# Kernel tuning notes

Hardware: AMD Instinct MI355X
Metric: run time of the kernel (lower is better)

The kernel has to match this reference:

```python
import jax, jax.numpy as jnp
import numpy as np

TOPK = 2
SCALE = 32.0 / 16.0  # alpha / rank
EPS = 1e-20


def setup_inputs() -> dict:
    key = jax.random.key(0)
    ks = jax.random.split(key, 6)
    B, S, D = 4, 4096, 2048
    E, R, QO, VO = 8, 16, 2048, 2048
    return {
        "hidden_states": jax.random.normal(ks[0], (B, S, D), dtype=jnp.float32),
        "router_weight": jax.random.normal(ks[1], (E, D), dtype=jnp.float32) * 0.02,
        "q_lora_a": jax.random.normal(ks[2], (E, D, R), dtype=jnp.float32) * 0.02,
        "q_lora_b": jax.random.normal(ks[3], (E, R, QO), dtype=jnp.float32) * 0.02,
        "v_lora_a": jax.random.normal(ks[4], (E, D, R), dtype=jnp.float32) * 0.02,
        "v_lora_b": jax.random.normal(ks[5], (E, R, VO), dtype=jnp.float32) * 0.02,
    }


def reference(hidden_states, router_weight, q_lora_a, q_lora_b, v_lora_a, v_lora_b):
    orig_shape = hidden_states.shape[:-1]
    D = hidden_states.shape[-1]
    E = router_weight.shape[0]
    h = hidden_states.reshape(-1, D)                       # [T, D]

    # --- routing ---
    logits = h @ router_weight.T                           # [T, E]
    probs = jax.nn.softmax(logits, axis=-1)
    scores, idx = jax.lax.top_k(probs, TOPK)               # [T, K]
    scores = scores / (jnp.sum(scores, axis=-1, keepdims=True) + EPS)
    # dense per-expert combine weight (0 for unselected experts), incl. LoRA scale
    w = jnp.sum(jax.nn.one_hot(idx, E, dtype=h.dtype) * scores[..., None], axis=1) * SCALE  # [T, E]

    # --- grouped LoRA (dense over experts; E and rank are small) ---
    q_low = jnp.einsum('td,edr->ter', h, q_lora_a) * w[:, :, None]  # [T, E, R]
    v_low = jnp.einsum('td,edr->ter', h, v_lora_a) * w[:, :, None]
    q_delta = jnp.einsum('ter,erq->tq', q_low, q_lora_b)            # [T, QO]
    v_delta = jnp.einsum('ter,erv->tv', v_low, v_lora_b)            # [T, VO]

    return (q_delta.reshape(*orig_shape, q_delta.shape[-1]),
            v_delta.reshape(*orig_shape, v_delta.shape[-1]))
```

## Files before the change

kernel.cpp:

```cpp
#include <hip/hip_runtime.h>

#define T_TOKENS 16384
#define DIM 2048
#define NE 8
#define QOUT 2048
#define LSCALE 2.0f

typedef __attribute__((ext_vector_type(4))) float f32x4;
typedef __attribute__((ext_vector_type(8))) short s16x8;
typedef __attribute__((ext_vector_type(4))) short s16x4;

__device__ __forceinline__ short f2bf(float f) {
  unsigned u = __builtin_bit_cast(unsigned, f);
  u += 0x7fffu + ((u >> 16) & 1u);
  return (short)(u >> 16);
}

__device__ __forceinline__ void barrier_lds() {
  asm volatile("s_waitcnt lgkmcnt(0)" ::: "memory");
  __builtin_amdgcn_s_barrier();
}

__global__ __launch_bounds__(256) void k_pack(
    const float* __restrict__ qa, const float* __restrict__ qb,
    const float* __restrict__ va, const float* __restrict__ vb,
    short* __restrict__ Bq1, short* __restrict__ Bv1,
    short* __restrict__ Bq2, short* __restrict__ Bv2) {
  int tid = blockIdx.x * 256 + threadIdx.x;
  if (tid < 65536) {
    int mat = tid >> 15;
    int idx = tid & 32767;
    int d8 = idx >> 7, c = idx & 127;
    int e = c >> 4, r = c & 15;
    const float* src = mat ? va : qa;
    short* dst = mat ? Bv1 : Bq1;
    s16x8 v;
#pragma unroll
    for (int j = 0; j < 8; ++j)
      v[j] = f2bf(src[((size_t)e * DIM + d8 * 8 + j) * 16 + r]);
    *(s16x8*)(dst + (size_t)idx * 8) = v;
  } else {
    int t2 = tid - 65536;
    int mat = t2 >> 15;
    int idx = t2 & 32767;
    int k8 = idx >> 11, c = idx & 2047;
    const float* src = mat ? vb : qb;
    short* dst = mat ? Bv2 : Bq2;
    s16x8 v;
#pragma unroll
    for (int j = 0; j < 8; ++j)
      v[j] = f2bf(src[(size_t)(k8 * 8 + j) * QOUT + c]);
    *(s16x8*)(dst + (size_t)idx * 8) = v;
  }
}

__global__ __launch_bounds__(512) void k_fused(
    const float* __restrict__ h, const float* __restrict__ rw,
    const short* __restrict__ Bq1, const short* __restrict__ Bv1,
    const short* __restrict__ Bq2, const short* __restrict__ Bv2,
    float* __restrict__ out) {
  __shared__ short At[2][32][72];
  __shared__ short low[32][264];
  __shared__ float wl[32][NE];

  const int tid = threadIdx.x;
  const int lane = tid & 63, wv = tid >> 6;
  const int lrow = lane & 15, lk = lane >> 4;
  const int row0 = blockIdx.x * 32;
  const int r  = tid >> 4;
  const int kq = (tid & 15) * 4;

  const float* hrow = h + (size_t)(row0 + r) * DIM + kq;
  const short* B1 = (wv >= 4) ? Bv1 : Bq1;
  int cc2[2];
#pragma unroll
  for (int ct = 0; ct < 2; ++ct) cc2[ct] = (wv & 3) * 32 + ct * 16 + lrow;

  float4 hv0 = *(const float4*)(hrow);
  float4 hv1 = *(const float4*)(hrow + 64);

  float lg[NE] = {0.f, 0.f, 0.f, 0.f, 0.f, 0.f, 0.f, 0.f};
  f32x4 acc1[2][2] = {};

#pragma unroll 2
  for (int kb = 0; kb < DIM; kb += 64) {
    const int cur = (kb >> 6) & 1;
    float4 hv2 = *(const float4*)(hrow + ((kb + 128) & (DIM - 1)));
    s16x8 bA[2], bB[2];
#pragma unroll
    for (int ct = 0; ct < 2; ++ct) {
      int d8 = (kb >> 3) + lk;
      bA[ct] = *(const s16x8*)(B1 + ((size_t)d8 * 128 + cc2[ct]) * 8);
      bB[ct] = *(const s16x8*)(B1 + ((size_t)(d8 + 4) * 128 + cc2[ct]) * 8);
    }
    s16x4 hb4;
    hb4[0] = f2bf(hv0.x); hb4[1] = f2bf(hv0.y);
    hb4[2] = f2bf(hv0.z); hb4[3] = f2bf(hv0.w);
    *(s16x4*)&At[cur][r][kq] = hb4;
#pragma unroll
    for (int e = 0; e < NE; ++e) {
      float4 rv = *(const float4*)(rw + e * DIM + kb + kq);
      lg[e] += hv0.x * rv.x + hv0.y * rv.y + hv0.z * rv.z + hv0.w * rv.w;
    }
    barrier_lds();
    s16x8 a0[2], a1[2];
#pragma unroll
    for (int rt = 0; rt < 2; ++rt) {
      a0[rt] = *(const s16x8*)&At[cur][rt * 16 + lrow][lk * 8];
      a1[rt] = *(const s16x8*)&At[cur][rt * 16 + lrow][32 + lk * 8];
    }
#pragma unroll
    for (int rt = 0; rt < 2; ++rt)
#pragma unroll
      for (int ct = 0; ct < 2; ++ct) {
        acc1[rt][ct] = __builtin_amdgcn_mfma_f32_16x16x32_bf16(bA[ct], a0[rt], acc1[rt][ct], 0, 0, 0);
        acc1[rt][ct] = __builtin_amdgcn_mfma_f32_16x16x32_bf16(bB[ct], a1[rt], acc1[rt][ct], 0, 0, 0);
      }
    hv0 = hv1; hv1 = hv2;
  }

#pragma unroll
  for (int e = 0; e < NE; ++e) {
    lg[e] += __shfl_xor(lg[e], 1, 64);
    lg[e] += __shfl_xor(lg[e], 2, 64);
    lg[e] += __shfl_xor(lg[e], 4, 64);
    lg[e] += __shfl_xor(lg[e], 8, 64);
  }
  float mx = lg[0];
#pragma unroll
  for (int e = 1; e < NE; ++e) mx = fmaxf(mx, lg[e]);
  float p[NE], sum = 0.f;
#pragma unroll
  for (int e = 0; e < NE; ++e) { p[e] = expf(lg[e] - mx); sum += p[e]; }
  int i1 = 0; float v1 = p[0];
#pragma unroll
  for (int e = 1; e < NE; ++e) if (p[e] > v1) { v1 = p[e]; i1 = e; }
  float v2 = -1.f; int i2 = 0;
#pragma unroll
  for (int e = 0; e < NE; ++e) if (e != i1 && p[e] > v2) { v2 = p[e]; i2 = e; }
  float s1 = v1 / sum, s2 = v2 / sum;
  float dn = s1 + s2 + 1e-20f;
  float w1 = s1 / dn * LSCALE, w2 = s2 / dn * LSCALE;
  if ((tid & 15) < 8) {
    int el = tid & 7;
    wl[r][el] = (el == i1) ? w1 : ((el == i2) ? w2 : 0.f);
  }

  const int m = wv >> 2;
  const int cwave = (wv & 3) * 512;
  const short* B2 = m ? Bv2 : Bq2;
  s16x8 bc[4];
#pragma unroll
  for (int ct = 0; ct < 4; ++ct) {
    int c = cwave + ct * 16 + lrow;
    bc[ct] = *(const s16x8*)(B2 + ((size_t)lk * QOUT + c) * 8);
  }

  __syncthreads();
#pragma unroll
  for (int rt = 0; rt < 2; ++rt)
#pragma unroll
    for (int ct = 0; ct < 2; ++ct) {
      int tok = rt * 16 + lrow;
      float wgt = wl[tok][(wv & 3) * 2 + ct];
      s16x4 v;
#pragma unroll
      for (int j = 0; j < 4; ++j) v[j] = f2bf(acc1[rt][ct][j] * wgt);
      *(s16x4*)&low[tok][wv * 32 + ct * 16 + lk * 4] = v;
    }
  barrier_lds();

  float* op = out + (size_t)m * T_TOKENS * QOUT;
  s16x8 a2[2][4];
#pragma unroll
  for (int rt = 0; rt < 2; ++rt)
#pragma unroll
    for (int kk = 0; kk < 4; ++kk)
      a2[rt][kk] = *(const s16x8*)&low[rt * 16 + lrow][m * 128 + kk * 32 + lk * 8];

  f32x4 acc[2][4] = {};
#pragma unroll 4
  for (int it = 0; it < 32; ++it) {
    const int sub = it >> 2, kk = it & 3;
    const int itn = (it + 1) & 31;
    const int subn = itn >> 2, kkn = itn & 3;
    s16x8 bn[4];
#pragma unroll
    for (int ct = 0; ct < 4; ++ct) {
      int c = cwave + subn * 64 + ct * 16 + lrow;
      bn[ct] = *(const s16x8*)(B2 + ((size_t)(kkn * 4 + lk) * QOUT + c) * 8);
    }
#pragma unroll
    for (int rt = 0; rt < 2; ++rt)
#pragma unroll
      for (int ct = 0; ct < 4; ++ct)
        acc[rt][ct] = __builtin_amdgcn_mfma_f32_16x16x32_bf16(bc[ct], a2[rt][kk], acc[rt][ct], 0, 0, 0);
    if (kk == 3) {
      int cb = cwave + sub * 64;
#pragma unroll
      for (int rt = 0; rt < 2; ++rt)
#pragma unroll
        for (int ct = 0; ct < 4; ++ct) {
          int t = row0 + rt * 16 + lrow;
          int col = cb + ct * 16 + lk * 4;
          __builtin_nontemporal_store(acc[rt][ct], (f32x4*)(op + (size_t)t * QOUT + col));
          acc[rt][ct] = (f32x4){0.f, 0.f, 0.f, 0.f};
        }
    }
#pragma unroll
    for (int ct = 0; ct < 4; ++ct) bc[ct] = bn[ct];
  }
}

extern "C" void kernel_launch(void* const* d_in, const int* in_sizes, int n_in,
                              void* d_out, int out_size, void* d_ws, size_t ws_size,
                              hipStream_t stream) {
  const float* h  = (const float*)d_in[0];
  const float* rw = (const float*)d_in[1];
  const float* qa = (const float*)d_in[2];
  const float* qb = (const float*)d_in[3];
  const float* va = (const float*)d_in[4];
  const float* vb = (const float*)d_in[5];
  float* out = (float*)d_out;
  char* ws = (char*)d_ws;

  short* Bq1 = (short*)(ws);
  short* Bv1 = (short*)(ws + (512 << 10));
  short* Bq2 = (short*)(ws + (1024 << 10));
  short* Bv2 = (short*)(ws + (1536 << 10));

  k_pack<<<512, 256, 0, stream>>>(qa, qb, va, vb, Bq1, Bv1, Bq2, Bv2);
  k_fused<<<T_TOKENS / 32, 512, 0, stream>>>(h, rw, Bq1, Bv1, Bq2, Bv2, out);
}
```

Measured before the change: 140.9 us.

## Stage hidden states into LDS via async global_load_lds with triple buffering

Replaces the register-prefetched float4 loads of hidden states with direct global-to-LDS async loads into a three-deep, XOR-swizzled fp32 LDS buffer. The bf16 conversion now happens after reading from LDS, and a vmcnt(1) barrier keeps one load in flight. The aim is to free registers and overlap the h stream with the MFMA work. The B2 preload also moves after the low-rank write, and the loop is no longer unrolled, which may cost some instruction overlap.

```diff
diff --git a/kernel.cpp b/kernel.cpp
--- a/kernel.cpp
+++ b/kernel.cpp
@@ -16,8 +16,26 @@
   return (short)(u >> 16);
 }
 
+__device__ __forceinline__ s16x8 pack8(float4 a, float4 b) {
+  s16x8 r;
+  r[0] = f2bf(a.x); r[1] = f2bf(a.y); r[2] = f2bf(a.z); r[3] = f2bf(a.w);
+  r[4] = f2bf(b.x); r[5] = f2bf(b.y); r[6] = f2bf(b.z); r[7] = f2bf(b.w);
+  return r;
+}
+
+__device__ __forceinline__ void gload16(const void* g, void* l) {
+  __builtin_amdgcn_global_load_lds(
+      (const __attribute__((address_space(1))) void*)g,
+      (__attribute__((address_space(3))) void*)l, 16, 0, 0);
+}
+
 __device__ __forceinline__ void barrier_lds() {
   asm volatile("s_waitcnt lgkmcnt(0)" ::: "memory");
+  __builtin_amdgcn_s_barrier();
+}
+
+__device__ __forceinline__ void barrier_vm1() {
+  asm volatile("s_waitcnt vmcnt(1) lgkmcnt(0)" ::: "memory");
   __builtin_amdgcn_s_barrier();
 }
 
@@ -59,7 +77,7 @@
     const short* __restrict__ Bq1, const short* __restrict__ Bv1,
     const short* __restrict__ Bq2, const short* __restrict__ Bv2,
     float* __restrict__ out) {
-  __shared__ short At[2][32][72];
+  __shared__ float Ah[3][32][64];
   __shared__ short low[32][264];
   __shared__ float wl[32][NE];
 
@@ -67,56 +85,61 @@
   const int lane = tid & 63, wv = tid >> 6;
   const int lrow = lane & 15, lk = lane >> 4;
   const int row0 = blockIdx.x * 32;
-  const int r  = tid >> 4;
-  const int kq = (tid & 15) * 4;
-
-  const float* hrow = h + (size_t)(row0 + r) * DIM + kq;
+  const int g_r = tid >> 4;
+  const int g_s = tid & 15;
+  const int psw = (g_s ^ (g_r & 15));
+
   const short* B1 = (wv >= 4) ? Bv1 : Bq1;
   int cc2[2];
 #pragma unroll
   for (int ct = 0; ct < 2; ++ct) cc2[ct] = (wv & 3) * 32 + ct * 16 + lrow;
 
-  float4 hv0 = *(const float4*)(hrow);
-  float4 hv1 = *(const float4*)(hrow + 64);
+  const float* hsrc = h + (size_t)(row0 + g_r) * DIM + psw * 4;
+
+  gload16(hsrc, (char*)&Ah[0][0][0] + wv * 1024);
+  gload16(hsrc + 64, (char*)&Ah[1][0][0] + wv * 1024);
+  barrier_vm1();
 
   float lg[NE] = {0.f, 0.f, 0.f, 0.f, 0.f, 0.f, 0.f, 0.f};
   f32x4 acc1[2][2] = {};
-
-#pragma unroll 2
+  int cur = 0, nxt = 1, nx2 = 2;
+
+#pragma unroll 1
   for (int kb = 0; kb < DIM; kb += 64) {
-    const int cur = (kb >> 6) & 1;
-    float4 hv2 = *(const float4*)(hrow + ((kb + 128) & (DIM - 1)));
-    s16x8 bA[2], bB[2];
-#pragma unroll
-    for (int ct = 0; ct < 2; ++ct) {
-      int d8 = (kb >> 3) + lk;
-      bA[ct] = *(const s16x8*)(B1 + ((size_t)d8 * 128 + cc2[ct]) * 8);
-      bB[ct] = *(const s16x8*)(B1 + ((size_t)(d8 + 4) * 128 + cc2[ct]) * 8);
-    }
-    s16x4 hb4;
-    hb4[0] = f2bf(hv0.x); hb4[1] = f2bf(hv0.y);
-    hb4[2] = f2bf(hv0.z); hb4[3] = f2bf(hv0.w);
-    *(s16x4*)&At[cur][r][kq] = hb4;
-#pragma unroll
-    for (int e = 0; e < NE; ++e) {
-      float4 rv = *(const float4*)(rw + e * DIM + kb + kq);
-      lg[e] += hv0.x * rv.x + hv0.y * rv.y + hv0.z * rv.z + hv0.w * rv.w;
-    }
-    barrier_lds();
-    s16x8 a0[2], a1[2];
+    float4 hv = *(const float4*)&Ah[cur][g_r][psw * 4];
+#pragma unroll 1
+    for (int g = 0; g < 2; ++g) {
+#pragma unroll
+      for (int e = 0; e < 4; ++e) {
+        float4 rv = *(const float4*)(rw + (g * 4 + e) * DIM + kb + g_s * 4);
+        lg[g * 4 + e] += hv.x * rv.x + hv.y * rv.y + hv.z * rv.z + hv.w * rv.w;
+      }
+    }
+    s16x8 b[2][2];
+#pragma unroll
+    for (int hf = 0; hf < 2; ++hf)
+#pragma unroll
+      for (int ct = 0; ct < 2; ++ct) {
+        int d8 = (kb >> 3) + hf * 4 + lk;
+        b[hf][ct] = *(const s16x8*)(B1 + ((size_t)d8 * 128 + cc2[ct]) * 8);
+      }
 #pragma unroll
     for (int rt = 0; rt < 2; ++rt) {
-      a0[rt] = *(const s16x8*)&At[cur][rt * 16 + lrow][lk * 8];
-      a1[rt] = *(const s16x8*)&At[cur][rt * 16 + lrow][32 + lk * 8];
-    }
-#pragma unroll
-    for (int rt = 0; rt < 2; ++rt)
-#pragma unroll
-      for (int ct = 0; ct < 2; ++ct) {
-        acc1[rt][ct] = __builtin_amdgcn_mfma_f32_16x16x32_bf16(bA[ct], a0[rt], acc1[rt][ct], 0, 0, 0);
-        acc1[rt][ct] = __builtin_amdgcn_mfma_f32_16x16x32_bf16(bB[ct], a1[rt], acc1[rt][ct], 0, 0, 0);
+      const float* base = &Ah[cur][rt * 16 + lrow][0];
+#pragma unroll
+      for (int hf = 0; hf < 2; ++hf) {
+        int s0 = hf * 8 + lk * 2;
+        float4 f0 = *(const float4*)(base + ((s0 ^ lrow) * 4));
+        float4 f1 = *(const float4*)(base + (((s0 + 1) ^ lrow) * 4));
+        s16x8 a = pack8(f0, f1);
+#pragma unroll
+        for (int ct = 0; ct < 2; ++ct)
+          acc1[rt][ct] = __builtin_amdgcn_mfma_f32_16x16x32_bf16(b[hf][ct], a, acc1[rt][ct], 0, 0, 0);
       }
-    hv0 = hv1; hv1 = hv2;
+    }
+    gload16(hsrc + ((kb + 128) & (DIM - 1)), (char*)&Ah[nx2][0][0] + wv * 1024);
+    barrier_vm1();
+    int t = cur; cur = nxt; nxt = nx2; nx2 = t;
   }
 
 #pragma unroll
@@ -141,22 +164,11 @@
   float s1 = v1 / sum, s2 = v2 / sum;
   float dn = s1 + s2 + 1e-20f;
   float w1 = s1 / dn * LSCALE, w2 = s2 / dn * LSCALE;
-  if ((tid & 15) < 8) {
-    int el = tid & 7;
-    wl[r][el] = (el == i1) ? w1 : ((el == i2) ? w2 : 0.f);
-  }
-
-  const int m = wv >> 2;
-  const int cwave = (wv & 3) * 512;
-  const short* B2 = m ? Bv2 : Bq2;
-  s16x8 bc[4];
-#pragma unroll
-  for (int ct = 0; ct < 4; ++ct) {
-    int c = cwave + ct * 16 + lrow;
-    bc[ct] = *(const s16x8*)(B2 + ((size_t)lk * QOUT + c) * 8);
-  }
-
-  __syncthreads();
+  if (g_s < 8) {
+    wl[g_r][g_s] = (g_s == i1) ? w1 : ((g_s == i2) ? w2 : 0.f);
+  }
+  barrier_lds();
+
 #pragma unroll
   for (int rt = 0; rt < 2; ++rt)
 #pragma unroll
@@ -170,7 +182,18 @@
     }
   barrier_lds();
 
+  const int m = wv >> 2;
+  const int cwave = (wv & 3) * 512;
+  const short* B2 = m ? Bv2 : Bq2;
   float* op = out + (size_t)m * T_TOKENS * QOUT;
+
+  s16x8 bc[4];
+#pragma unroll
+  for (int ct = 0; ct < 4; ++ct) {
+    int c = cwave + ct * 16 + lrow;
+    bc[ct] = *(const s16x8*)(B2 + ((size_t)lk * QOUT + c) * 8);
+  }
+
   s16x8 a2[2][4];
 #pragma unroll
   for (int rt = 0; rt < 2; ++rt)
```

Result: slower. 160.8 us (+14.1%).
